# Optimization experiments

Hardware: AMD Instinct MI355X
Metric: run time of the kernel (lower is better)

## Reference

```python
import jax, jax.numpy as jnp
import numpy as np
from jax import lax

B, DIM, DIM_OUT, NH = 8, 512, 512, 8
HD = DIM_OUT // NH          # 64, also the depthwise-conv channel count
SQ, SKV = (1, 1), (2, 2)    # stride_q, stride_kv
PAD = 1                      # kernel 3 -> padding 3//2
SCALE = HD ** -0.5
EPS = 1e-6


def _dw_conv(x, w, stride):
    # x: [N, C, H, W], w: [C, 1, kh, kw]; depthwise conv (groups = C), no bias
    return lax.conv_general_dilated(
        x, w, window_strides=stride, padding=[(PAD, PAD), (PAD, PAD)],
        dimension_numbers=('NCHW', 'OIHW', 'NCHW'),
        feature_group_count=x.shape[1])


def _ln(x, w, b):
    m = jnp.mean(x, -1, keepdims=True)
    v = jnp.var(x, -1, keepdims=True)
    return (x - m) * lax.rsqrt(v + EPS) * w + b


def _pool(t, w, stride, ln_w, ln_b, H, W):
    # t: [B, NH, 1+H*W, HD] with cls token at index 0
    Bn = t.shape[0]
    cls = t[:, :, :1, :]
    body = t[:, :, 1:, :].reshape(Bn * NH, H, W, HD).transpose(0, 3, 1, 2)
    body = _dw_conv(body, w, stride)
    ph, pw = body.shape[2], body.shape[3]
    body = body.reshape(Bn, NH, HD, ph * pw).transpose(0, 1, 3, 2)
    out = jnp.concatenate([cls, body], axis=2)
    return _ln(out, ln_w, ln_b), (ph, pw)


def _rel_bias(r_q4, q_shape, k_shape, rel_pos_h, rel_pos_w):
    # r_q4: [B, NH, q_h*q_w, HD] (cls token stripped)
    q_h, q_w = q_shape
    k_h, k_w = k_shape

    def dist(qs, ks):
        qr, kr = max(ks / qs, 1.0), max(qs / ks, 1.0)
        d = np.arange(qs)[:, None] * qr - np.arange(ks)[None, :] * kr + (ks - 1) * kr
        return d.astype(np.int64)

    Rh = rel_pos_h[dist(q_h, k_h)]  # [q_h, k_h, HD]
    Rw = rel_pos_w[dist(q_w, k_w)]  # [q_w, k_w, HD]
    r_q = r_q4.reshape(r_q4.shape[0], NH, q_h, q_w, HD)
    rel_h = jnp.einsum('byhwc,hkc->byhwk', r_q, Rh)  # [B,NH,q_h,q_w,k_h]
    rel_w = jnp.einsum('byhwc,wkc->byhwk', r_q, Rw)  # [B,NH,q_h,q_w,k_w]
    return rel_h[..., :, None] + rel_w[..., None, :]  # [B,NH,q_h,q_w,k_h,k_w]


def setup_inputs() -> dict:
    key = jax.random.key(0)
    ks = jax.random.split(key, 16)
    H = W = 56
    N = H * W + 1
    rel_dim = 2 * H - 1  # 111
    return {
        'x': jax.random.normal(ks[0], (B, N, DIM), jnp.float32),
        'qkv_w': jax.random.normal(ks[1], (3 * DIM_OUT, DIM), jnp.float32) * DIM ** -0.5,
        'qkv_b': jax.random.normal(ks[2], (3 * DIM_OUT,), jnp.float32) * 0.02,
        'proj_w': jax.random.normal(ks[3], (DIM_OUT, DIM_OUT), jnp.float32) * DIM_OUT ** -0.5,
        'proj_b': jax.random.normal(ks[4], (DIM_OUT,), jnp.float32) * 0.02,
        'pool_q_w': jax.random.normal(ks[5], (HD, 1, 3, 3), jnp.float32) / 3.0,
        'pool_k_w': jax.random.normal(ks[6], (HD, 1, 3, 3), jnp.float32) / 3.0,
        'pool_v_w': jax.random.normal(ks[7], (HD, 1, 3, 3), jnp.float32) / 3.0,
        'lnq_w': 1.0 + 0.1 * jax.random.normal(ks[8], (HD,), jnp.float32),
        'lnq_b': 0.02 * jax.random.normal(ks[9], (HD,), jnp.float32),
        'lnk_w': 1.0 + 0.1 * jax.random.normal(ks[10], (HD,), jnp.float32),
        'lnk_b': 0.02 * jax.random.normal(ks[11], (HD,), jnp.float32),
        'lnv_w': 1.0 + 0.1 * jax.random.normal(ks[12], (HD,), jnp.float32),
        'lnv_b': 0.02 * jax.random.normal(ks[13], (HD,), jnp.float32),
        'rel_pos_h': 0.02 * jax.random.normal(ks[14], (rel_dim, HD), jnp.float32),
        'rel_pos_w': 0.02 * jax.random.normal(ks[15], (rel_dim, HD), jnp.float32),
        'hw_h': 56,
        'hw_w': 56,
    }


def reference(x, qkv_w, qkv_b, proj_w, proj_b, pool_q_w, pool_k_w, pool_v_w,
              lnq_w, lnq_b, lnk_w, lnk_b, lnv_w, lnv_b, rel_pos_h, rel_pos_w,
              hw_h, hw_w):
    Bn, N, _ = x.shape
    qkv = (x @ qkv_w.T + qkv_b).reshape(Bn, N, 3, NH, HD).transpose(2, 0, 3, 1, 4)
    q, k, v = qkv[0], qkv[1], qkv[2]  # each [B, NH, N, HD]
    q, q_shape = _pool(q, pool_q_w, SQ, lnq_w, lnq_b, hw_h, hw_w)
    k, k_shape = _pool(k, pool_k_w, SKV, lnk_w, lnk_b, hw_h, hw_w)
    v, _ = _pool(v, pool_v_w, SKV, lnv_w, lnv_b, hw_h, hw_w)
    attn = (q * SCALE) @ k.swapaxes(-2, -1)  # [B, NH, Nq, Nk]
    q_h, q_w = q_shape
    k_h, k_w = k_shape
    bias = _rel_bias(q[:, :, 1:, :], q_shape, k_shape, rel_pos_h, rel_pos_w)
    blk = attn[:, :, 1:, 1:].reshape(Bn, NH, q_h, q_w, k_h, k_w) + bias
    attn = attn.at[:, :, 1:, 1:].set(blk.reshape(Bn, NH, q_h * q_w, k_h * k_w))
    attn = jax.nn.softmax(attn, axis=-1)
    out = attn @ v                                   # [B, NH, Nq, HD]
    out = out.at[:, :, 1:, :].add(q[:, :, 1:, :])    # residual on non-cls rows
    out = out.transpose(0, 2, 1, 3).reshape(Bn, -1, DIM_OUT)
    return out @ proj_w.T + proj_b
```

## Files before the change

### kernel.cpp

```cpp
#include <hip/hip_runtime.h>
#include <hip/hip_bf16.h>
#include <cstdint>
#include <cstddef>

#define BB 8
#define NHH 8
#define NQ 3137
#define NKV 785
#define HDIM 64
#define AUG 128
#define MROWS (BB*NQ)
#define SCALE 0.125f
#define VTP 832

typedef unsigned short ushort_t;
typedef __attribute__((ext_vector_type(8))) short s16x8;
typedef __attribute__((ext_vector_type(4))) float f32x4;
typedef __attribute__((ext_vector_type(16))) float f32x16;

__device__ __forceinline__ float bf2f(ushort_t u) {
  union { unsigned int i; float f; } v; v.i = ((unsigned int)u) << 16; return v.f;
}
__device__ __forceinline__ ushort_t f2bf(float f) {
  union { float f; unsigned int i; } v; v.f = f;
  unsigned int r = v.i + 0x7fffu + ((v.i >> 16) & 1u);
  return (ushort_t)(r >> 16);
}
__device__ __forceinline__ unsigned int cvt_pk_bf16(float lo, float hi) {
  unsigned int r;
  asm("v_cvt_pk_bf16_f32 %0, %1, %2" : "=v"(r) : "v"(lo), "v"(hi));
  return r;
}
__device__ __forceinline__ s16x8 lds_frag8(const ushort_t* base, int row, int slot) {
  const char* p = (const char*)base + row * 128 + (((slot ^ (row & 7)) & 7) << 4);
  return *(const s16x8*)p;
}
__device__ __forceinline__ s16x8 lds_frag16(const ushort_t* base, int row, int slot) {
  const char* p = (const char*)base + row * 256 + (((slot ^ (row & 15)) & 15) << 4);
  return *(const s16x8*)p;
}

template<int EPI, bool AF32, bool WF32>
__global__ __launch_bounds__(256) void mfma_gemm_bt(
    const void* __restrict__ Ap, const void* __restrict__ Wp,
    const float* __restrict__ bias, void* __restrict__ outp, int M) {
  __shared__ ushort_t As[128][40];
  __shared__ ushort_t Bs[128][40];
  const int tid = threadIdx.x;
  const int l = tid & 63, w = tid >> 6;
  const int wr = w >> 1, wc = w & 1;
  const int lrow = l & 15, lk = l >> 4;
  const int m0 = blockIdx.y * 128, n0 = blockIdx.x * 128;
  const int srow = tid >> 2, sch = tid & 3;
  const int mA0 = m0 + srow      < M ? m0 + srow      : M - 1;
  const int mA1 = m0 + 64 + srow < M ? m0 + 64 + srow : M - 1;
  const size_t ar0 = (size_t)mA0 * 512, ar1 = (size_t)mA1 * 512;
  const size_t br0 = (size_t)(n0 + srow) * 512, br1 = (size_t)(n0 + 64 + srow) * 512;
  const ushort_t* Ab = (const ushort_t*)Ap;
  const float*    Af = (const float*)Ap;
  const ushort_t* Wb = (const ushort_t*)Wp;
  const float*    Wf = (const float*)Wp;
  auto ld8 = [&](const ushort_t* pb, const float* pf, size_t ofs, bool f32) -> uint4 {
    if (!f32) return *(const uint4*)(pb + ofs);
    const float4 v0 = *(const float4*)(pf + ofs);
    const float4 v1 = *(const float4*)(pf + ofs + 4);
    uint4 r;
    r.x = cvt_pk_bf16(v0.x, v0.y); r.y = cvt_pk_bf16(v0.z, v0.w);
    r.z = cvt_pk_bf16(v1.x, v1.y); r.w = cvt_pk_bf16(v1.z, v1.w);
    return r;
  };
  f32x4 acc[4][4];
  #pragma unroll
  for (int i = 0; i < 4; ++i) {
    #pragma unroll
    for (int j = 0; j < 4; ++j) acc[i][j] = (f32x4){0.f, 0.f, 0.f, 0.f};
  }
  for (int k0 = 0; k0 < 512; k0 += 32) {
    const uint4 a0 = ld8(Ab, Af, ar0 + k0 + sch * 8, AF32);
    const uint4 a1 = ld8(Ab, Af, ar1 + k0 + sch * 8, AF32);
    const uint4 b0 = ld8(Wb, Wf, br0 + k0 + sch * 8, WF32);
    const uint4 b1 = ld8(Wb, Wf, br1 + k0 + sch * 8, WF32);
    __syncthreads();
    *(uint4*)(&As[srow][sch * 8])      = a0;
    *(uint4*)(&As[64 + srow][sch * 8]) = a1;
    *(uint4*)(&Bs[srow][sch * 8])      = b0;
    *(uint4*)(&Bs[64 + srow][sch * 8]) = b1;
    __syncthreads();
    s16x8 af[4], bfr[4];
    #pragma unroll
    for (int mi = 0; mi < 4; ++mi)
      af[mi] = *(const s16x8*)(&As[wr * 64 + mi * 16 + lrow][lk * 8]);
    #pragma unroll
    for (int ni = 0; ni < 4; ++ni)
      bfr[ni] = *(const s16x8*)(&Bs[wc * 64 + ni * 16 + lrow][lk * 8]);
    #pragma unroll
    for (int mi = 0; mi < 4; ++mi) {
      #pragma unroll
      for (int ni = 0; ni < 4; ++ni)
        acc[mi][ni] = __builtin_amdgcn_mfma_f32_16x16x32_bf16(
            af[mi], bfr[ni], acc[mi][ni], 0, 0, 0);
    }
  }
  #pragma unroll
  for (int mi = 0; mi < 4; ++mi) {
    #pragma unroll
    for (int r = 0; r < 4; ++r) {
      const int m = m0 + wr * 64 + mi * 16 + 4 * lk + r;
      if (m >= M) continue;
      #pragma unroll
      for (int ni = 0; ni < 4; ++ni) {
        const int n = n0 + wc * 64 + ni * 16 + lrow;
        const float v = acc[mi][ni][r] + bias[n];
        if (EPI == 0) {
          const int which = n >> 9, y = (n >> 6) & 7, c = n & 63;
          const int b_ = m / NQ, tok = m - b_ * NQ;
          ((ushort_t*)outp)[((((size_t)which * BB + b_) * NHH + y) * NQ + tok) * HDIM + c] = f2bf(v);
        } else {
          ((float*)outp)[(size_t)m * 512 + n] = v;
        }
      }
    }
  }
}

template<int MODE>
__global__ __launch_bounds__(256) void pool_ln_kernel(
    const ushort_t* __restrict__ in, ushort_t* __restrict__ out0,
    ushort_t* __restrict__ out1,
    const float* __restrict__ cw, const float* __restrict__ lnw,
    const float* __restrict__ lnb, int stride, int OW, int R) {
  const int tid = threadIdx.x;
  const int c = tid & 63;
  const int rid = blockIdx.x * 4 + (tid >> 6);
  const int by = rid / R;
  const int n = rid - by * R;
  const ushort_t* ibase = in + (size_t)by * NQ * HDIM;
  float val;
  if (n == 0) {
    val = bf2f(ibase[c]);
  } else {
    const int p = n - 1;
    const int ho = p / OW, wo = p - ho * OW;
    float s = 0.f;
    #pragma unroll
    for (int dh = 0; dh < 3; ++dh) {
      const int hh = ho * stride + dh - 1;
      if (hh < 0 || hh >= 56) continue;
      #pragma unroll
      for (int dw = 0; dw < 3; ++dw) {
        const int ww = wo * stride + dw - 1;
        if (ww < 0 || ww >= 56) continue;
        s += cw[c * 9 + dh * 3 + dw] * bf2f(ibase[(size_t)(1 + hh * 56 + ww) * HDIM + c]);
      }
    }
    val = s;
  }
  float sum = val, sq = val * val;
  #pragma unroll
  for (int off = 32; off > 0; off >>= 1) {
    sum += __shfl_xor(sum, off);
    sq  += __shfl_xor(sq,  off);
  }
  const float mean = sum * (1.f / 64.f);
  const float var  = sq * (1.f / 64.f) - mean * mean;
  const float rs = rsqrtf(var + 1e-6f);
  const float lno = (val - mean) * rs * lnw[c] + lnb[c];
  if (MODE == 0) {
    out0[(size_t)rid * HDIM + c] = f2bf(lno);
  } else if (MODE == 1) {
    out0[(size_t)rid * HDIM + c] = f2bf(lno);
    out1[(size_t)rid * AUG + c] = f2bf(lno * SCALE);
    out1[(size_t)rid * AUG + 64 + c] = 0;
  } else {
    out0[(size_t)rid * AUG + c] = f2bf(lno);
    ushort_t aug = 0;
    if (n >= 1) {
      const int p = n - 1;
      const int kh = p / 28, kw = p - 28 * kh;
      if (c < 28) { if (c == kh) aug = 0x3F80; }
      else if (c < 56) { if (c - 28 == kw) aug = 0x3F80; }
    }
    out0[(size_t)rid * AUG + 64 + c] = aug;
  }
}

__global__ __launch_bounds__(256) void transpose_v_kernel(
    const ushort_t* __restrict__ vin, ushort_t* __restrict__ vtout) {
  __shared__ ushort_t T[64][65];
  const int tid = threadIdx.x;
  const int by = blockIdx.y;
  const int n0 = blockIdx.x * 64;
  #pragma unroll
  for (int half = 0; half < 2; ++half) {
    const int idx = tid + half * 256;
    const int r = idx >> 3, s = idx & 7;
    const int n = n0 + r;
    uint4 d = make_uint4(0u, 0u, 0u, 0u);
    if (n < NKV) d = *(const uint4*)(vin + ((size_t)by * NKV + n) * HDIM + s * 8);
    const ushort_t* dp = (const ushort_t*)&d;
    #pragma unroll
    for (int e = 0; e < 8; ++e) T[r][s * 8 + e] = dp[e];
  }
  __syncthreads();
  #pragma unroll
  for (int half = 0; half < 2; ++half) {
    const int idx = tid + half * 256;
    const int c = idx >> 3, g = idx & 7;
    ushort_t pk[8];
    #pragma unroll
    for (int e = 0; e < 8; ++e) pk[e] = T[g * 8 + e][c];
    *(uint4*)(vtout + ((size_t)by * 64 + c) * VTP + n0 + g * 8) = *(const uint4*)pk;
  }
}

__global__ __launch_bounds__(256) void relbias_mfma_kernel(
    const ushort_t* __restrict__ qb, const float* __restrict__ rph,
    const float* __restrict__ rpw, ushort_t* __restrict__ qaug) {
  const int tid = threadIdx.x;
  const int l = tid & 63, w = tid >> 6;
  const int lrow = l & 15, lk = l >> 4;
  const int hw = blockIdx.y;
  const int mode = blockIdx.z;
  const int r0 = blockIdx.x * 256 + w * 64;
  const float* tab = mode ? rpw : rph;
  s16x8 bfr[2][2];
  #pragma unroll
  for (int ni = 0; ni < 2; ++ni) {
    const int kh = ni * 16 + lrow;
    int trow = hw - 2 * kh + 54;
    if (trow < 0) trow = 0;
    const float* tr = tab + (size_t)trow * 64 + lk * 8;
    #pragma unroll
    for (int k0 = 0; k0 < 2; ++k0) {
      const float4 t0 = *(const float4*)(tr + k0 * 32);
      const float4 t1 = *(const float4*)(tr + k0 * 32 + 4);
      s16x8 bb;
      bb[0] = (short)f2bf(t0.x); bb[1] = (short)f2bf(t0.y);
      bb[2] = (short)f2bf(t0.z); bb[3] = (short)f2bf(t0.w);
      bb[4] = (short)f2bf(t1.x); bb[5] = (short)f2bf(t1.y);
      bb[6] = (short)f2bf(t1.z); bb[7] = (short)f2bf(t1.w);
      bfr[ni][k0] = bb;
    }
  }
  s16x8 af[4][2];
  #pragma unroll
  for (int mi = 0; mi < 4; ++mi) {
    const int rA = r0 + mi * 16 + lrow;
    const int by = rA / 56, oth = rA - 56 * by;
    const int tok = mode ? (1 + oth * 56 + hw) : (1 + hw * 56 + oth);
    const ushort_t* qp = qb + ((size_t)by * NQ + tok) * HDIM + lk * 8;
    af[mi][0] = *(const s16x8*)(qp);
    af[mi][1] = *(const s16x8*)(qp + 32);
  }
  f32x4 acc[4][2];
  #pragma unroll
  for (int mi = 0; mi < 4; ++mi) {
    #pragma unroll
    for (int ni = 0; ni < 2; ++ni) acc[mi][ni] = (f32x4){0.f, 0.f, 0.f, 0.f};
  }
  #pragma unroll
  for (int k0 = 0; k0 < 2; ++k0) {
    #pragma unroll
    for (int mi = 0; mi < 4; ++mi) {
      #pragma unroll
      for (int ni = 0; ni < 2; ++ni)
        acc[mi][ni] = __builtin_amdgcn_mfma_f32_16x16x32_bf16(
            af[mi][k0], bfr[ni][k0], acc[mi][ni], 0, 0, 0);
    }
  }
  const int augofs = 64 + mode * 28;
  #pragma unroll
  for (int mi = 0; mi < 4; ++mi) {
    #pragma unroll
    for (int r = 0; r < 4; ++r) {
      const int row = r0 + mi * 16 + 4 * lk + r;
      const int by = row / 56, oth = row - 56 * by;
      const int tok = 1 + (mode ? (oth * 56 + hw) : (hw * 56 + oth));
      ushort_t* orow = qaug + ((size_t)by * NQ + tok) * AUG + augofs;
      #pragma unroll
      for (int ni = 0; ni < 2; ++ni) {
        const int kh = ni * 16 + lrow;
        if (kh < 28) orow[kh] = f2bf(acc[mi][ni][r]);
      }
    }
  }
}

__global__ __launch_bounds__(256) void attn_mfma32_kernel(
    const ushort_t* __restrict__ qaug, const ushort_t* __restrict__ kaug,
    const ushort_t* __restrict__ qb, const ushort_t* __restrict__ vt,
    ushort_t* __restrict__ outp) {
  __shared__ ushort_t Kl[2][64 * AUG];
  __shared__ ushort_t Vl[2][64 * 64];
  const int tid = threadIdx.x;
  const int l = tid & 63;
  const int w = tid >> 6;
  const int h = l >> 5, q5 = l & 31;
  const int by = blockIdx.y;
  const int qt0 = blockIdx.x * 128;
  const int qloc = w * 32 + q5;
  const int qglob = qt0 + qloc;
  const int qcl = qglob < NQ ? qglob : NQ - 1;
  const ushort_t* qrow = qaug + ((size_t)by * NQ + qcl) * AUG;
  s16x8 qf[8];
  #pragma unroll
  for (int cb = 0; cb < 8; ++cb)
    qf[cb] = *(const s16x8*)(qrow + cb * 16 + h * 8);
  f32x16 ot0, ot1;
  #pragma unroll
  for (int i = 0; i < 16; ++i) { ot0[i] = 0.f; ot1[i] = 0.f; }
  float mr = -1e30f, lr = 0.f;
  const int krow = tid >> 2, ks4 = (tid & 3) * 4;
  const int vrow = tid >> 3, vslot = tid & 7;
  const ushort_t* kbase = kaug + (size_t)by * NKV * AUG + ks4 * 8;
  const ushort_t* vbase0 = vt + ((size_t)by * 64 + vrow) * VTP + vslot * 8;
  const ushort_t* vbase1 = vt + ((size_t)by * 64 + vrow + 32) * VTP + vslot * 8;
  uint4 kreg[4], vreg[2];
  auto load_tile = [&](int j0) {
    int jK = j0 + krow; if (jK > NKV - 1) jK = NKV - 1;
    const ushort_t* ksrc = kbase + (size_t)jK * AUG;
    kreg[0] = *(const uint4*)(ksrc);
    kreg[1] = *(const uint4*)(ksrc + 8);
    kreg[2] = *(const uint4*)(ksrc + 16);
    kreg[3] = *(const uint4*)(ksrc + 24);
    vreg[0] = *(const uint4*)(vbase0 + j0);
    vreg[1] = *(const uint4*)(vbase1 + j0);
  };
  auto store_tile = [&](int buf) {
    char* kb_ = (char*)&Kl[buf][0] + krow * 256;
    const int rm = krow & 15;
    *(uint4*)(kb_ + (((ks4 + 0) ^ rm) << 4)) = kreg[0];
    *(uint4*)(kb_ + (((ks4 + 1) ^ rm) << 4)) = kreg[1];
    *(uint4*)(kb_ + (((ks4 + 2) ^ rm) << 4)) = kreg[2];
    *(uint4*)(kb_ + (((ks4 + 3) ^ rm) << 4)) = kreg[3];
    *(uint4*)((char*)&Vl[buf][0] + vrow * 128 + (((vslot ^ (vrow & 7)) & 7) << 4)) = vreg[0];
    *(uint4*)((char*)&Vl[buf][0] + (vrow + 32) * 128 + (((vslot ^ ((vrow + 32) & 7)) & 7) << 4)) = vreg[1];
  };
  load_tile(0);
  store_tile(0);
  load_tile(64);
  #pragma unroll 1
  for (int it = 0; it < 13; ++it) {
    const int cur = it & 1;
    const ushort_t* Kc = &Kl[cur][0];
    const ushort_t* Vc = &Vl[cur][0];
    __syncthreads();
    f32x16 st0, st1;
    #pragma unroll
    for (int i = 0; i < 16; ++i) { st0[i] = 0.f; st1[i] = 0.f; }
    __builtin_amdgcn_s_setprio(1);
    #pragma unroll
    for (int cb = 0; cb < 8; ++cb) {
      st0 = __builtin_amdgcn_mfma_f32_32x32x16_bf16(
          lds_frag16(Kc, q5, cb * 2 + h), qf[cb], st0, 0, 0, 0);
      st1 = __builtin_amdgcn_mfma_f32_32x32x16_bf16(
          lds_frag16(Kc, 32 + q5, cb * 2 + h), qf[cb], st1, 0, 0, 0);
    }
    __builtin_amdgcn_s_setprio(0);
    float pa[16], pb[16];
    #pragma unroll
    for (int r = 0; r < 16; ++r) { pa[r] = st0[r]; pb[r] = st1[r]; }
    if (it == 12) {
      #pragma unroll
      for (int r = 0; r < 16; ++r) {
        const int klocal = (r & 3) + 8 * (r >> 2) + 4 * h;
        if (768 + klocal >= NKV) pa[r] = -1e30f;
        pb[r] = -1e30f;
      }
    }
    float mloc = pa[0];
    #pragma unroll
    for (int r = 1; r < 16; ++r) mloc = fmaxf(mloc, pa[r]);
    #pragma unroll
    for (int r = 0; r < 16; ++r) mloc = fmaxf(mloc, pb[r]);
    mloc = fmaxf(mloc, __shfl_xor(mloc, 32));
    if (!__all(mloc <= mr + 8.f)) {
      const float mn = fmaxf(mr, mloc);
      const float sc = __expf(mr - mn);
      mr = mn;
      lr *= sc;
      #pragma unroll
      for (int i = 0; i < 16; ++i) { ot0[i] *= sc; ot1[i] *= sc; }
    }
    float ps = 0.f;
    #pragma unroll
    for (int r = 0; r < 16; ++r) { pa[r] = __expf(pa[r] - mr); ps += pa[r]; }
    #pragma unroll
    for (int r = 0; r < 16; ++r) { pb[r] = __expf(pb[r] - mr); ps += pb[r]; }
    ps += __shfl_xor(ps, 32);
    lr += ps;
    auto pvstep = [&](const float (&pv)[16], int kt) {
      #pragma unroll
      for (int kbk = 0; kbk < 2; ++kbk) {
        const unsigned int pk01 = cvt_pk_bf16(pv[kbk * 8 + 0], pv[kbk * 8 + 1]);
        const unsigned int pk23 = cvt_pk_bf16(pv[kbk * 8 + 2], pv[kbk * 8 + 3]);
        const unsigned int pk45 = cvt_pk_bf16(pv[kbk * 8 + 4], pv[kbk * 8 + 5]);
        const unsigned int pk67 = cvt_pk_bf16(pv[kbk * 8 + 6], pv[kbk * 8 + 7]);
        const unsigned int sA = (unsigned int)__shfl_xor((int)pk01, 32);
        const unsigned int sB = (unsigned int)__shfl_xor((int)pk45, 32);
        const unsigned int sC = (unsigned int)__shfl_xor((int)pk23, 32);
        const unsigned int sD = (unsigned int)__shfl_xor((int)pk67, 32);
        int4 fw;
        fw.x = (int)(h ? sB : pk01);
        fw.y = (int)(h ? sD : pk23);
        fw.z = (int)(h ? pk45 : sA);
        fw.w = (int)(h ? pk67 : sC);
        s16x8 pf;
        __builtin_memcpy(&pf, &fw, 16);
        const int slot = kt * 4 + kbk * 2 + h;
        __builtin_amdgcn_s_setprio(1);
        ot0 = __builtin_amdgcn_mfma_f32_32x32x16_bf16(
            lds_frag8(Vc, q5, slot), pf, ot0, 0, 0, 0);
        ot1 = __builtin_amdgcn_mfma_f32_32x32x16_bf16(
            lds_frag8(Vc, 32 + q5, slot), pf, ot1, 0, 0, 0);
        __builtin_amdgcn_s_setprio(0);
      }
    };
    pvstep(pa, 0);
    pvstep(pb, 1);
    if (it < 12) {
      store_tile(cur ^ 1);
      if (it < 11) load_tile((it + 2) * 64);
    }
  }
  const float inv = 1.f / lr;
  if (qglob < NQ) {
    const int b_ = by >> 3, y_ = by & 7;
    ushort_t* obase = outp + ((size_t)b_ * NQ + qglob) * 512 + (size_t)y_ * 64;
    const ushort_t* rbase = qb + ((size_t)by * NQ + qglob) * HDIM;
    #pragma unroll
    for (int ch = 0; ch < 2; ++ch) {
      #pragma unroll
      for (int rg = 0; rg < 4; ++rg) {
        const int c0 = ch * 32 + 8 * rg + 4 * h;
        float vv[4];
        #pragma unroll
        for (int e = 0; e < 4; ++e)
          vv[e] = (ch ? ot1[rg * 4 + e] : ot0[rg * 4 + e]) * inv;
        if (qglob > 0) {
          #pragma unroll
          for (int e = 0; e < 4; ++e) vv[e] += bf2f(rbase[c0 + e]);
        }
        ushort_t pk[4] = { f2bf(vv[0]), f2bf(vv[1]), f2bf(vv[2]), f2bf(vv[3]) };
        *(uint2*)(obase + c0) = *(const uint2*)pk;
      }
    }
  }
}

extern "C" void kernel_launch(void* const* d_in, const int* in_sizes, int n_in,
                              void* d_out, int out_size, void* d_ws, size_t ws_size,
                              hipStream_t stream) {
  const float* x        = (const float*)d_in[0];
  const float* qkv_w    = (const float*)d_in[1];
  const float* qkv_b    = (const float*)d_in[2];
  const float* proj_w   = (const float*)d_in[3];
  const float* proj_b   = (const float*)d_in[4];
  const float* pool_q_w = (const float*)d_in[5];
  const float* pool_k_w = (const float*)d_in[6];
  const float* pool_v_w = (const float*)d_in[7];
  const float* lnq_w    = (const float*)d_in[8];
  const float* lnq_b    = (const float*)d_in[9];
  const float* lnk_w    = (const float*)d_in[10];
  const float* lnk_b    = (const float*)d_in[11];
  const float* lnv_w    = (const float*)d_in[12];
  const float* lnv_b    = (const float*)d_in[13];
  const float* rel_pos_h = (const float*)d_in[14];
  const float* rel_pos_w = (const float*)d_in[15];

  constexpr size_t E1 = (size_t)BB * NHH * NQ * HDIM;
  char* ws = (char*)d_ws;
  size_t off = 0;
  ushort_t* qkv_raw = (ushort_t*)(ws + off); off += 3 * E1 * 2;
  ushort_t* q_bf    = (ushort_t*)(ws + off); off += E1 * 2;
  ushort_t* qaug    = (ushort_t*)(ws + off); off += (size_t)BB * NHH * NQ * AUG * 2;
  ushort_t* kaug    = (ushort_t*)(ws + off); off += (size_t)BB * NHH * NKV * AUG * 2;
  ushort_t* v_bf    = (ushort_t*)(ws + off); off += (size_t)BB * NHH * NKV * HDIM * 2;
  ushort_t* v_t     = (ushort_t*)(ws + off); off += (size_t)64 * 64 * VTP * 2;
  ushort_t* attn_bf = qkv_raw;

  mfma_gemm_bt<0, true, true><<<dim3(12, 197), 256, 0, stream>>>(
      x, qkv_w, qkv_b, (void*)qkv_raw, MROWS);

  pool_ln_kernel<1><<<(64 * NQ) / 4,  256, 0, stream>>>(qkv_raw,          q_bf, qaug, pool_q_w, lnq_w, lnq_b, 1, 56, NQ);
  pool_ln_kernel<2><<<(64 * NKV) / 4, 256, 0, stream>>>(qkv_raw + E1,     kaug, nullptr, pool_k_w, lnk_w, lnk_b, 2, 28, NKV);
  pool_ln_kernel<0><<<(64 * NKV) / 4, 256, 0, stream>>>(qkv_raw + 2 * E1, v_bf, nullptr, pool_v_w, lnv_w, lnv_b, 2, 28, NKV);

  transpose_v_kernel<<<dim3(13, 64), 256, 0, stream>>>(v_bf, v_t);

  relbias_mfma_kernel<<<dim3(14, 56, 2), 256, 0, stream>>>(q_bf, rel_pos_h, rel_pos_w, qaug);

  attn_mfma32_kernel<<<dim3(25, 64), 256, 0, stream>>>(qaug, kaug, q_bf, v_t, attn_bf);

  mfma_gemm_bt<1, false, true><<<dim3(4, 197), 256, 0, stream>>>(
      attn_bf, proj_w, proj_b, d_out, MROWS);
}
```

Measured before the change: 546.7 us.

## Single-buffer K/V shared tiles in attention kernel to halve LDS use

Replaces the double-buffered K and V shared-memory tiles with a single buffer. Each iteration now stores the prefetched registers, synchronizes, then issues the next global load before computing. The separate pa/pb float copies are dropped and the work is done in place on the MFMA accumulators, which lowers register pressure. Halving LDS aims to allow more resident blocks per CU, at the cost of an extra barrier per iteration and less overlap between LDS writes and compute.

```diff
diff --git a/kernel.cpp b/kernel.cpp
--- a/kernel.cpp
+++ b/kernel.cpp
@@ -290,8 +290,8 @@
     const ushort_t* __restrict__ qaug, const ushort_t* __restrict__ kaug,
     const ushort_t* __restrict__ qb, const ushort_t* __restrict__ vt,
     ushort_t* __restrict__ outp) {
-  __shared__ ushort_t Kl[2][64 * AUG];
-  __shared__ ushort_t Vl[2][64 * 64];
+  __shared__ ushort_t Kl[64 * AUG];
+  __shared__ ushort_t Vl[64 * 64];
   const int tid = threadIdx.x;
   const int l = tid & 63;
   const int w = tid >> 6;
@@ -326,25 +326,23 @@
     vreg[0] = *(const uint4*)(vbase0 + j0);
     vreg[1] = *(const uint4*)(vbase1 + j0);
   };
-  auto store_tile = [&](int buf) {
-    char* kb_ = (char*)&Kl[buf][0] + krow * 256;
+  auto store_tile = [&]() {
+    char* kb_ = (char*)Kl + krow * 256;
     const int rm = krow & 15;
     *(uint4*)(kb_ + (((ks4 + 0) ^ rm) << 4)) = kreg[0];
     *(uint4*)(kb_ + (((ks4 + 1) ^ rm) << 4)) = kreg[1];
     *(uint4*)(kb_ + (((ks4 + 2) ^ rm) << 4)) = kreg[2];
     *(uint4*)(kb_ + (((ks4 + 3) ^ rm) << 4)) = kreg[3];
-    *(uint4*)((char*)&Vl[buf][0] + vrow * 128 + (((vslot ^ (vrow & 7)) & 7) << 4)) = vreg[0];
-    *(uint4*)((char*)&Vl[buf][0] + (vrow + 32) * 128 + (((vslot ^ ((vrow + 32) & 7)) & 7) << 4)) = vreg[1];
+    *(uint4*)((char*)Vl + vrow * 128 + (((vslot ^ (vrow & 7)) & 7) << 4)) = vreg[0];
+    *(uint4*)((char*)Vl + (vrow + 32) * 128 + (((vslot ^ ((vrow + 32) & 7)) & 7) << 4)) = vreg[1];
   };
   load_tile(0);
-  store_tile(0);
-  load_tile(64);
   #pragma unroll 1
   for (int it = 0; it < 13; ++it) {
-    const int cur = it & 1;
-    const ushort_t* Kc = &Kl[cur][0];
-    const ushort_t* Vc = &Vl[cur][0];
     __syncthreads();
+    store_tile();
+    __syncthreads();
+    if (it < 12) load_tile((it + 1) * 64);
     f32x16 st0, st1;
     #pragma unroll
     for (int i = 0; i < 16; ++i) { st0[i] = 0.f; st1[i] = 0.f; }
@@ -352,27 +350,24 @@
     #pragma unroll
     for (int cb = 0; cb < 8; ++cb) {
       st0 = __builtin_amdgcn_mfma_f32_32x32x16_bf16(
-          lds_frag16(Kc, q5, cb * 2 + h), qf[cb], st0, 0, 0, 0);
+          lds_frag16(Kl, q5, cb * 2 + h), qf[cb], st0, 0, 0, 0);
       st1 = __builtin_amdgcn_mfma_f32_32x32x16_bf16(
-          lds_frag16(Kc, 32 + q5, cb * 2 + h), qf[cb], st1, 0, 0, 0);
+          lds_frag16(Kl, 32 + q5, cb * 2 + h), qf[cb], st1, 0, 0, 0);
     }
     __builtin_amdgcn_s_setprio(0);
-    float pa[16], pb[16];
-    #pragma unroll
-    for (int r = 0; r < 16; ++r) { pa[r] = st0[r]; pb[r] = st1[r]; }
     if (it == 12) {
       #pragma unroll
       for (int r = 0; r < 16; ++r) {
         const int klocal = (r & 3) + 8 * (r >> 2) + 4 * h;
-        if (768 + klocal >= NKV) pa[r] = -1e30f;
-        pb[r] = -1e30f;
-      }
-    }
-    float mloc = pa[0];
-    #pragma unroll
-    for (int r = 1; r < 16; ++r) mloc = fmaxf(mloc, pa[r]);
-    #pragma unroll
-    for (int r = 0; r < 16; ++r) mloc = fmaxf(mloc, pb[r]);
+        if (768 + klocal >= NKV) st0[r] = -1e30f;
+        st1[r] = -1e30f;
+      }
+    }
+    float mloc = st0[0];
+    #pragma unroll
+    for (int r = 1; r < 16; ++r) mloc = fmaxf(mloc, st0[r]);
+    #pragma unroll
+    for (int r = 0; r < 16; ++r) mloc = fmaxf(mloc, st1[r]);
     mloc = fmaxf(mloc, __shfl_xor(mloc, 32));
     if (!__all(mloc <= mr + 8.f)) {
       const float mn = fmaxf(mr, mloc);
@@ -384,12 +379,12 @@
     }
     float ps = 0.f;
     #pragma unroll
-    for (int r = 0; r < 16; ++r) { pa[r] = __expf(pa[r] - mr); ps += pa[r]; }
-    #pragma unroll
-    for (int r = 0; r < 16; ++r) { pb[r] = __expf(pb[r] - mr); ps += pb[r]; }
+    for (int r = 0; r < 16; ++r) { st0[r] = __expf(st0[r] - mr); ps += st0[r]; }
+    #pragma unroll
+    for (int r = 0; r < 16; ++r) { st1[r] = __expf(st1[r] - mr); ps += st1[r]; }
     ps += __shfl_xor(ps, 32);
     lr += ps;
-    auto pvstep = [&](const float (&pv)[16], int kt) {
+    auto pvstep = [&](const f32x16& pv, int kt) {
       #pragma unroll
       for (int kbk = 0; kbk < 2; ++kbk) {
         const unsigned int pk01 = cvt_pk_bf16(pv[kbk * 8 + 0], pv[kbk * 8 + 1]);
@@ -410,18 +405,14 @@
         const int slot = kt * 4 + kbk * 2 + h;
         __builtin_amdgcn_s_setprio(1);
         ot0 = __builtin_amdgcn_mfma_f32_32x32x16_bf16(
-            lds_frag8(Vc, q5, slot), pf, ot0, 0, 0, 0);
+            lds_frag8(Vl, q5, slot), pf, ot0, 0, 0, 0);
         ot1 = __builtin_amdgcn_mfma_f32_32x32x16_bf16(
-            lds_frag8(Vc, 32 + q5, slot), pf, ot1, 0, 0, 0);
+            lds_frag8(Vl, 32 + q5, slot), pf, ot1, 0, 0, 0);
         __builtin_amdgcn_s_setprio(0);
       }
     };
-    pvstep(pa, 0);
-    pvstep(pb, 1);
-    if (it < 12) {
-      store_tile(cur ^ 1);
-      if (it < 11) load_tile((it + 2) * 64);
-    }
+    pvstep(st0, 0);
+    pvstep(st1, 1);
   }
   const float inv = 1.f / lr;
   if (qglob < NQ) {
```

Measured after the change: 556.0 us. Within noise of the previous version (+1.7%).
